# Kernel optimization log

Hardware: AMD Instinct MI355X
Metric: run time of the kernel (lower is better)

Reference implementation:

```python
import jax, jax.numpy as jnp
import numpy as np

EPS = 1e-10
N_NODES = 100000
OUT_CH = 128
N_EDGES = 625000


def setup_inputs() -> dict:
    key = jax.random.key(0)
    k_emb, k_eidx, k_enorm, k_lw, k_sw = jax.random.split(key, 5)
    emb = jax.random.normal(k_emb, (N_NODES, OUT_CH), dtype=jnp.float32) * 0.02
    edge_index = jax.random.randint(k_eidx, (2, N_EDGES), 0, N_NODES, dtype=jnp.int64)
    edge_norm = jax.random.uniform(k_enorm, (N_EDGES,), dtype=jnp.float32)
    scale = 1.0 / np.sqrt(OUT_CH)
    loc_w = jax.random.normal(k_lw, (OUT_CH, OUT_CH), dtype=jnp.float32) * scale
    loc_b = jnp.zeros((OUT_CH,), dtype=jnp.float32)
    std_w = jax.random.normal(k_sw, (OUT_CH, OUT_CH), dtype=jnp.float32) * scale
    std_b = jnp.zeros((OUT_CH,), dtype=jnp.float32)
    return {"emb": emb, "edge_index": edge_index, "edge_norm": edge_norm,
            "loc_w": loc_w, "loc_b": loc_b, "std_w": std_w, "std_b": std_b}


def reference(emb, edge_index, edge_norm, loc_w, loc_b, std_w, std_b):
    """GraphEncoder (GraphConv gather-scale-scatter + Linear loc/std) followed by
    GraphDecoder dot-product logits on the same edge list. Eval mode: z = loc."""
    sidx = edge_index[0]
    tidx = edge_index[1]
    # GraphConv: message = x[sidx] * enorm ; scatter_add into target nodes
    message = emb[sidx] * edge_norm[:, None]               # [E, C]
    ptr = jax.ops.segment_sum(message, tidx, num_segments=emb.shape[0])  # [N, C]
    # Encoder heads (torch Linear: x @ W.T + b)
    loc = ptr @ loc_w.T + loc_b                            # [N, C]
    std = jax.nn.softplus(ptr @ std_w.T + std_b) + EPS     # [N, C]
    z = loc  # eval-mode embedding
    # GraphDecoder: Bernoulli logits per edge
    logits = jnp.sum(z[sidx] * z[tidx], axis=1)            # [E]
    return loc, std, logits
```

## Files before the change

### kernel.cpp

```cpp
#include <hip/hip_runtime.h>

#define N_NODES 100000
#define OUT_CH  128
#define N_EDGES 625000
#define NB_SCAN 98

typedef short short8 __attribute__((ext_vector_type(8)));
typedef float f32x4  __attribute__((ext_vector_type(4)));
typedef float f32x2  __attribute__((ext_vector_type(2)));
typedef unsigned u32x4 __attribute__((ext_vector_type(4)));

__device__ inline short f32_bf16(float f) {
    union { float f; unsigned u; } c{f};
    unsigned r = 0x7FFFu + ((c.u >> 16) & 1u);
    return (short)((c.u + r) >> 16);
}
__device__ inline unsigned pack_bf16x2(float lo, float hi) {
    return (unsigned)(unsigned short)f32_bf16(lo) |
           ((unsigned)(unsigned short)f32_bf16(hi) << 16);
}
__device__ inline float sp_fast(float x) {
    float e = __expf(-fabsf(x));
    return fmaxf(x, 0.f) + __logf(1.f + e);
}

#if defined(__has_builtin)
#if __has_builtin(__builtin_amdgcn_cvt_pk_f32_fp8) && __has_builtin(__builtin_amdgcn_cvt_pk_fp8_f32)
#define HWFP8 1
#endif
#endif
#ifndef HWFP8
#define HWFP8 0
#endif

__device__ inline unsigned f32_fp8_manual(float f) {
    union { float fl; unsigned u; } c{f};
    unsigned s = (c.u >> 31) << 7;
    float af = fabsf(f);
    if (!(af < 448.f)) return s | 0x7E;
    if (af < 0.015625f) {
        unsigned q = (unsigned)__float2int_rn(af * 512.f);
        return s | q;
    }
    unsigned u = c.u;
    u += 0x7FFFF + ((u >> 20) & 1);
    int e = (int)((u >> 23) & 255) - 127;
    if (e > 8) return s | 0x7E;
    return s | (((unsigned)(e + 7)) << 3) | ((u >> 20) & 7);
}
__device__ inline float fp8_f32_manual(unsigned b) {
    unsigned s = (b >> 7) & 1, e = (b >> 3) & 15, m = b & 7;
    if (e) { union { unsigned u; float f; } c{(s << 31) | ((e + 120) << 23) | (m << 20)}; return c.f; }
    float v = (float)m * 0.001953125f;
    return s ? -v : v;
}

template <bool HI>
__device__ inline f32x2 fp8x2_f32(unsigned v) {
#if HWFP8
    return __builtin_amdgcn_cvt_pk_f32_fp8((int)v, HI);
#else
    unsigned sh = HI ? 16 : 0;
    f32x2 r;
    r.x = fp8_f32_manual((v >> sh) & 0xff);
    r.y = fp8_f32_manual((v >> (sh + 8)) & 0xff);
    return r;
#endif
}
template <bool HI>
__device__ inline unsigned fp8_pack2(float a, float b, unsigned old) {
#if HWFP8
    return (unsigned)__builtin_amdgcn_cvt_pk_fp8_f32(a, b, (int)old, HI);
#else
    unsigned v = f32_fp8_manual(a) | (f32_fp8_manual(b) << 8);
    return HI ? ((old & 0x0000ffffu) | (v << 16)) : ((old & 0xffff0000u) | v);
#endif
}

#define NBB 16
#define NBE 6250
#define NBH 2442
__global__ void prep_all(const float* __restrict__ lw, const float* __restrict__ sw,
                         short8* __restrict__ B, const float4* __restrict__ emb,
                         uint2* __restrict__ embf8, const int* __restrict__ ei,
                         int* __restrict__ counts, int use_fp8) {
    int bid = blockIdx.x, tid = threadIdx.x;
    if (bid < NBB) {
        int g = bid * 256 + tid;
        int lane = g & 63, nt = (g >> 6) & 15, ks = g >> 10;
        int c = nt * 16 + (lane & 15);
        int k = ks * 32 + (lane >> 4) * 8;
        const float* src = (c < OUT_CH) ? (lw + c * OUT_CH + k)
                                        : (sw + (c - OUT_CH) * OUT_CH + k);
        short8 o;
#pragma unroll
        for (int j = 0; j < 8; ++j) o[j] = f32_bf16(src[j]);
        B[(ks * 16 + nt) * 64 + lane] = o;
    } else if (bid < NBB + NBE) {
        if (!use_fp8) return;
        int i = (bid - NBB) * 256 + tid;
        float4 a = emb[2 * i], b = emb[2 * i + 1];
        unsigned lo = fp8_pack2<false>(a.x * 64.f, a.y * 64.f, 0u);
        lo = fp8_pack2<true>(a.z * 64.f, a.w * 64.f, lo);
        unsigned hi = fp8_pack2<false>(b.x * 64.f, b.y * 64.f, 0u);
        hi = fp8_pack2<true>(b.z * 64.f, b.w * 64.f, hi);
        uint2 o; o.x = lo; o.y = hi;
        embf8[i] = o;
    } else {
        int e = (bid - NBB - NBE) * 256 + tid;
        if (e < N_EDGES) atomicAdd(&counts[ei[N_EDGES + e]], 1);
    }
}

__global__ void scan1_k(const int* __restrict__ counts, int* __restrict__ offsets,
                        int* __restrict__ partials, int* __restrict__ cursors) {
    __shared__ int wsum[16];
    int tid = threadIdx.x, lane = tid & 63, wid = tid >> 6;
    int e = blockIdx.x * 1024 + tid;
    int v = (e < N_NODES) ? counts[e] : 0;
    int incl = v;
#pragma unroll
    for (int d = 1; d < 64; d <<= 1) {
        int t = __shfl_up(incl, d);
        if (lane >= d) incl += t;
    }
    if (lane == 63) wsum[wid] = incl;
    __syncthreads();
    if (wid == 0) {
        int w = (lane < 16) ? wsum[lane] : 0;
        int wi = w;
#pragma unroll
        for (int d = 1; d < 16; d <<= 1) {
            int t = __shfl_up(wi, d);
            if (lane >= d) wi += t;
        }
        if (lane < 16) wsum[lane] = wi - w;
        if (lane == 15) partials[blockIdx.x] = wi;
    }
    __syncthreads();
    int excl = incl - v + wsum[wid];
    if (e < N_NODES) { offsets[e] = excl; cursors[e] = excl; }
}

__global__ void scan2_k(int* __restrict__ partials, int nb) {
    int lane = threadIdx.x;
    int i0 = 2 * lane, i1 = 2 * lane + 1;
    int v0 = (i0 < nb) ? partials[i0] : 0;
    int v1 = (i1 < nb) ? partials[i1] : 0;
    int s = v0 + v1;
    int incl = s;
#pragma unroll
    for (int d = 1; d < 64; d <<= 1) {
        int t = __shfl_up(incl, d);
        if (lane >= d) incl += t;
    }
    int excl = incl - s;
    if (i0 < nb) partials[i0] = excl;
    if (i1 < nb) partials[i1] = excl + v0;
}

__global__ void reorder_k(const int* __restrict__ ei, const float* __restrict__ en,
                          const int* __restrict__ partials, int* __restrict__ cursors,
                          int4* __restrict__ edata, float nscale) {
    int e = blockIdx.x * blockDim.x + threadIdx.x;
    if (e >= N_EDGES) return;
    int t = ei[N_EDGES + e];
    int pos = partials[t >> 10] + atomicAdd(&cursors[t], 1);
    int4 d;
    d.x = ei[e];
    d.y = __float_as_int(en[e] * nscale);
    d.z = e;
    d.w = t;
    edata[pos] = d;
}

__global__ void gather_fp8_k(const unsigned short* __restrict__ embf8,
                             const int* __restrict__ offsets,
                             const int* __restrict__ partials,
                             const int4* __restrict__ edata,
                             unsigned* __restrict__ ptrb) {
    int g = blockIdx.x * blockDim.x + threadIdx.x;
    int node = __builtin_amdgcn_readfirstlane(g >> 6);
    int lane = threadIdx.x & 63;
    if (node >= N_NODES) return;
    int beg = offsets[node] + partials[node >> 10];
    int end = (node == N_NODES - 1) ? N_EDGES
              : offsets[node + 1] + partials[(node + 1) >> 10];
    float ax = 0.f, ay = 0.f;
    int j = beg;
    for (; j + 4 <= end; j += 4) {
        int4 p0 = edata[j], p1 = edata[j + 1], p2 = edata[j + 2], p3 = edata[j + 3];
        unsigned v0 = embf8[(size_t)p0.x * 64 + lane];
        unsigned v1 = embf8[(size_t)p1.x * 64 + lane];
        unsigned v2 = embf8[(size_t)p2.x * 64 + lane];
        unsigned v3 = embf8[(size_t)p3.x * 64 + lane];
        float n0f = __int_as_float(p0.y), n1f = __int_as_float(p1.y);
        float n2f = __int_as_float(p2.y), n3f = __int_as_float(p3.y);
        f32x2 d0 = fp8x2_f32<false>(v0), d1 = fp8x2_f32<false>(v1);
        f32x2 d2 = fp8x2_f32<false>(v2), d3 = fp8x2_f32<false>(v3);
        ax += d0.x * n0f + d1.x * n1f + d2.x * n2f + d3.x * n3f;
        ay += d0.y * n0f + d1.y * n1f + d2.y * n2f + d3.y * n3f;
    }
    for (; j < end; ++j) {
        int4 p = edata[j];
        float nm = __int_as_float(p.y);
        f32x2 d = fp8x2_f32<false>(embf8[(size_t)p.x * 64 + lane]);
        ax += d.x * nm; ay += d.y * nm;
    }
    ptrb[(size_t)node * 64 + lane] = pack_bf16x2(ax, ay);
}

__global__ void gather_f32_k(const float* __restrict__ emb,
                             const int* __restrict__ offsets,
                             const int* __restrict__ partials,
                             const int4* __restrict__ edata,
                             unsigned* __restrict__ ptrb) {
    int g = blockIdx.x * blockDim.x + threadIdx.x;
    int node = __builtin_amdgcn_readfirstlane(g >> 6);
    int lane = threadIdx.x & 63;
    if (node >= N_NODES) return;
    int beg = offsets[node] + partials[node >> 10];
    int end = (node == N_NODES - 1) ? N_EDGES
              : offsets[node + 1] + partials[(node + 1) >> 10];
    float ax = 0.f, ay = 0.f;
    const float2* base = (const float2*)emb;
    int j = beg;
    for (; j + 4 <= end; j += 4) {
        int4 p0 = edata[j], p1 = edata[j + 1], p2 = edata[j + 2], p3 = edata[j + 3];
        float2 v0 = base[(size_t)p0.x * 64 + lane];
        float2 v1 = base[(size_t)p1.x * 64 + lane];
        float2 v2 = base[(size_t)p2.x * 64 + lane];
        float2 v3 = base[(size_t)p3.x * 64 + lane];
        float n0f = __int_as_float(p0.y), n1f = __int_as_float(p1.y);
        float n2f = __int_as_float(p2.y), n3f = __int_as_float(p3.y);
        ax += v0.x * n0f + v1.x * n1f + v2.x * n2f + v3.x * n3f;
        ay += v0.y * n0f + v1.y * n1f + v2.y * n2f + v3.y * n3f;
    }
    for (; j < end; ++j) {
        int4 p = edata[j];
        float nm = __int_as_float(p.y);
        float2 v = base[(size_t)p.x * 64 + lane];
        ax += v.x * nm; ay += v.y * nm;
    }
    ptrb[(size_t)node * 64 + lane] = pack_bf16x2(ax, ay);
}

__global__ __launch_bounds__(256) void gemm_k(const short* __restrict__ P,
                                              float* __restrict__ out,
                                              const short8* __restrict__ B,
                                              const float* __restrict__ lb,
                                              const float* __restrict__ sb,
                                              unsigned* __restrict__ zf8, int write_z) {
    int tid = threadIdx.x;
    int wave = tid >> 6, lane = tid & 63;
    int n0 = (blockIdx.x * 4 + wave) * 16;
    if (n0 >= N_NODES) return;

    float* loc  = out;
    float* stdo = out + (size_t)N_NODES * OUT_CH;

    int prow = n0 + (lane & 15);
    int kb = (lane >> 4) * 8;

    f32x4 acc[16];
#pragma unroll
    for (int i = 0; i < 16; ++i) acc[i] = (f32x4)(0.f);

#pragma unroll
    for (int ks = 0; ks < 4; ++ks) {
        short8 a = *(const short8*)(P + (size_t)prow * OUT_CH + ks * 32 + kb);
#pragma unroll
        for (int nt = 0; nt < 16; ++nt) {
            short8 w = B[(ks * 16 + nt) * 64 + lane];
            acc[nt] = __builtin_amdgcn_mfma_f32_16x16x32_bf16(w, a, acc[nt], 0, 0, 0);
        }
    }

    int node = n0 + (lane & 15);
    int ch4 = (lane >> 4) * 4;
    float* lrow = loc  + (size_t)node * OUT_CH;
    float* srow = stdo + (size_t)node * OUT_CH;
    unsigned* zrow = zf8 + (size_t)node * 32;

#pragma unroll
    for (int nt = 0; nt < 8; ++nt) {
        int c = nt * 16 + ch4;
        float4 b4 = *(const float4*)(lb + c);
        float4 v;
        v.x = acc[nt][0] + b4.x; v.y = acc[nt][1] + b4.y;
        v.z = acc[nt][2] + b4.z; v.w = acc[nt][3] + b4.w;
        *(float4*)(lrow + c) = v;
        if (write_z) {
            unsigned zp = fp8_pack2<false>(v.x * 16.f, v.y * 16.f, 0u);
            zp = fp8_pack2<true>(v.z * 16.f, v.w * 16.f, zp);
            zrow[c >> 2] = zp;
        }
    }
#pragma unroll
    for (int nt = 8; nt < 16; ++nt) {
        int cc = nt * 16 + ch4 - OUT_CH;
        float4 b4 = *(const float4*)(sb + cc);
        float4 v;
        v.x = sp_fast(acc[nt][0] + b4.x) + 1e-10f;
        v.y = sp_fast(acc[nt][1] + b4.y) + 1e-10f;
        v.z = sp_fast(acc[nt][2] + b4.z) + 1e-10f;
        v.w = sp_fast(acc[nt][3] + b4.w) + 1e-10f;
        *(float4*)(srow + cc) = v;
    }
}

__global__ void logits_fp8_k(const u32x4* __restrict__ zf8,
                             const int4* __restrict__ edata,
                             float* __restrict__ lg) {
    int idx = blockIdx.x * blockDim.x + threadIdx.x;
    int p = idx >> 3, q = idx & 7;
    if (p >= N_EDGES) return;
    int4 md = edata[p];
    u32x4 a = zf8[(size_t)md.x * 8 + q];
    u32x4 b = zf8[(size_t)md.w * 8 + q];
    float d = 0.f;
#pragma unroll
    for (int k = 0; k < 4; ++k) {
        f32x2 al = fp8x2_f32<false>(a[k]), ah = fp8x2_f32<true>(a[k]);
        f32x2 bl = fp8x2_f32<false>(b[k]), bh = fp8x2_f32<true>(b[k]);
        d += al.x * bl.x + al.y * bl.y + ah.x * bh.x + ah.y * bh.y;
    }
#pragma unroll
    for (int m = 4; m >= 1; m >>= 1) d += __shfl_xor(d, m);
    if (q == 0) lg[md.z] = d * 0.00390625f;
}

__global__ void logits_f32_k(const float* __restrict__ z, const int* __restrict__ ei,
                             float* __restrict__ lg) {
    int idx = blockIdx.x * blockDim.x + threadIdx.x;
    int e = idx >> 5, q = idx & 31;
    if (e >= N_EDGES) return;
    int s = ei[e], t = ei[N_EDGES + e];
    float4 a = *(const float4*)(z + (size_t)s * OUT_CH + q * 4);
    float4 b = *(const float4*)(z + (size_t)t * OUT_CH + q * 4);
    float d = a.x * b.x + a.y * b.y + a.z * b.z + a.w * b.w;
#pragma unroll
    for (int m = 16; m >= 1; m >>= 1) d += __shfl_xor(d, m);
    if (q == 0) lg[e] = d;
}

extern "C" void kernel_launch(void* const* d_in, const int* in_sizes, int n_in,
                              void* d_out, int out_size, void* d_ws, size_t ws_size,
                              hipStream_t stream) {
    const float* emb = (const float*)d_in[0];
    const int*   ei  = (const int*)d_in[1];
    const float* en  = (const float*)d_in[2];
    const float* lw  = (const float*)d_in[3];
    const float* lb  = (const float*)d_in[4];
    const float* sw  = (const float*)d_in[5];
    const float* sb  = (const float*)d_in[6];
    float* out = (float*)d_out;

    char* ws = (char*)d_ws;
    size_t o = 0;
    short8* B       = (short8*)(ws + o); o += 65536;
    int*    counts  = (int*)(ws + o);    o += 400128;
    int*    offsets = (int*)(ws + o);    o += 400128;
    int*    cursors = (int*)(ws + o);    o += 400128;
    int*    partials= (int*)(ws + o);    o += 1024;
    int4*   edata   = (int4*)(ws + o);   o += (size_t)N_EDGES * 16;
    unsigned* ptrb  = (unsigned*)(ws + o); o += (size_t)N_NODES * OUT_CH * 2;

    unsigned* zf8   = (unsigned*)(ws + o);
    unsigned short* embf8 = (unsigned short*)(ws + o + (size_t)N_NODES * OUT_CH);
    size_t o_end = o + (size_t)N_NODES * OUT_CH * 2;
    int use_fp8 = (o_end <= ws_size) ? 1 : 0;

    hipMemsetAsync(counts, 0, N_NODES * sizeof(int), stream);

    prep_all<<<NBB + NBE + NBH, 256, 0, stream>>>(lw, sw, B, (const float4*)emb,
                                                  (uint2*)embf8, ei, counts, use_fp8);
    scan1_k<<<NB_SCAN, 1024, 0, stream>>>(counts, offsets, partials, cursors);
    scan2_k<<<1, 64, 0, stream>>>(partials, NB_SCAN);
    reorder_k<<<(N_EDGES + 255) / 256, 256, 0, stream>>>(
        ei, en, partials, cursors, edata, use_fp8 ? 0.015625f : 1.0f);
    if (use_fp8)
        gather_fp8_k<<<(N_NODES * 64 + 255) / 256, 256, 0, stream>>>(
            embf8, offsets, partials, edata, ptrb);
    else
        gather_f32_k<<<(N_NODES * 64 + 255) / 256, 256, 0, stream>>>(
            emb, offsets, partials, edata, ptrb);
    gemm_k<<<(N_NODES / 16 + 3) / 4, 256, 0, stream>>>((const short*)ptrb, out, B,
                                                       lb, sb, zf8, use_fp8);
    float* lg = out + (size_t)2 * N_NODES * OUT_CH;
    if (use_fp8)
        logits_fp8_k<<<((size_t)N_EDGES * 8 + 255) / 256, 256, 0, stream>>>(
            (const u32x4*)zf8, edata, lg);
    else
        logits_f32_k<<<((size_t)N_EDGES * 32 + 255) / 256, 256, 0, stream>>>(out, ei, lg);
}
```

Before: 185.8 us.

## Fuse fp8 neighbor gather with loc/std GEMM through shared memory

Merges the per-node fp8 gather and the bf16 MFMA projection into one kernel. Each 1024-thread block gathers 16 nodes, one per wave, into padded LDS rows, then each of the 16 waves computes one 16-column output tile and writes loc, std and the fp8 z copy. This removes the bf16 intermediate round trip through global memory and one kernel launch. In exchange it adds a block-wide barrier behind the slowest node's gather, and the large blocks may reduce occupancy flexibility.

```diff
diff --git a/kernel.cpp b/kernel.cpp
--- a/kernel.cpp
+++ b/kernel.cpp
@@ -4,6 +4,7 @@
 #define OUT_CH  128
 #define N_EDGES 625000
 #define NB_SCAN 98
+#define ROWD 68
 
 typedef short short8 __attribute__((ext_vector_type(8)));
 typedef float f32x4  __attribute__((ext_vector_type(4)));
@@ -174,15 +175,16 @@
     edata[pos] = d;
 }
 
-__global__ void gather_fp8_k(const unsigned short* __restrict__ embf8,
-                             const int* __restrict__ offsets,
-                             const int* __restrict__ partials,
-                             const int4* __restrict__ edata,
-                             unsigned* __restrict__ ptrb) {
-    int g = blockIdx.x * blockDim.x + threadIdx.x;
-    int node = __builtin_amdgcn_readfirstlane(g >> 6);
-    int lane = threadIdx.x & 63;
-    if (node >= N_NODES) return;
+__global__ __launch_bounds__(1024) void enc_fp8_k(
+        const unsigned short* __restrict__ embf8,
+        const int* __restrict__ offsets, const int* __restrict__ partials,
+        const int4* __restrict__ edata, const short8* __restrict__ B,
+        const float* __restrict__ lb, const float* __restrict__ sb,
+        float* __restrict__ out, unsigned* __restrict__ zf8) {
+    __shared__ unsigned lds[16 * ROWD];
+    int tid = threadIdx.x, wid = tid >> 6, lane = tid & 63;
+    int node = __builtin_amdgcn_readfirstlane(blockIdx.x * 16 + wid);
+
     int beg = offsets[node] + partials[node >> 10];
     int end = (node == N_NODES - 1) ? N_EDGES
               : offsets[node + 1] + partials[(node + 1) >> 10];
@@ -207,7 +209,39 @@
         f32x2 d = fp8x2_f32<false>(embf8[(size_t)p.x * 64 + lane]);
         ax += d.x * nm; ay += d.y * nm;
     }
-    ptrb[(size_t)node * 64 + lane] = pack_bf16x2(ax, ay);
+    lds[wid * ROWD + lane] = pack_bf16x2(ax, ay);
+    __syncthreads();
+
+    int arow = lane & 15, hi = lane >> 4;
+    f32x4 acc = (f32x4)(0.f);
+#pragma unroll
+    for (int ks = 0; ks < 4; ++ks) {
+        short8 a = *(const short8*)&lds[arow * ROWD + ks * 16 + hi * 4];
+        short8 w = B[(ks * 16 + wid) * 64 + lane];
+        acc = __builtin_amdgcn_mfma_f32_16x16x32_bf16(w, a, acc, 0, 0, 0);
+    }
+    int onode = blockIdx.x * 16 + arow;
+    int ch4 = hi * 4;
+    if (wid < 8) {
+        int c = wid * 16 + ch4;
+        float4 b4 = *(const float4*)(lb + c);
+        float4 v;
+        v.x = acc[0] + b4.x; v.y = acc[1] + b4.y;
+        v.z = acc[2] + b4.z; v.w = acc[3] + b4.w;
+        *(float4*)(out + (size_t)onode * OUT_CH + c) = v;
+        unsigned zp = fp8_pack2<false>(v.x * 16.f, v.y * 16.f, 0u);
+        zp = fp8_pack2<true>(v.z * 16.f, v.w * 16.f, zp);
+        zf8[(size_t)onode * 32 + (c >> 2)] = zp;
+    } else {
+        int cc = (wid - 8) * 16 + ch4;
+        float4 b4 = *(const float4*)(sb + cc);
+        float4 v;
+        v.x = sp_fast(acc[0] + b4.x) + 1e-10f;
+        v.y = sp_fast(acc[1] + b4.y) + 1e-10f;
+        v.z = sp_fast(acc[2] + b4.z) + 1e-10f;
+        v.w = sp_fast(acc[3] + b4.w) + 1e-10f;
+        *(float4*)(out + (size_t)N_NODES * OUT_CH + (size_t)onode * OUT_CH + cc) = v;
+    }
 }
 
 __global__ void gather_f32_k(const float* __restrict__ emb,
@@ -249,8 +283,7 @@
                                               float* __restrict__ out,
                                               const short8* __restrict__ B,
                                               const float* __restrict__ lb,
-                                              const float* __restrict__ sb,
-                                              unsigned* __restrict__ zf8, int write_z) {
+                                              const float* __restrict__ sb) {
     int tid = threadIdx.x;
     int wave = tid >> 6, lane = tid & 63;
     int n0 = (blockIdx.x * 4 + wave) * 16;
@@ -280,7 +313,6 @@
     int ch4 = (lane >> 4) * 4;
     float* lrow = loc  + (size_t)node * OUT_CH;
     float* srow = stdo + (size_t)node * OUT_CH;
-    unsigned* zrow = zf8 + (size_t)node * 32;
 
 #pragma unroll
     for (int nt = 0; nt < 8; ++nt) {
@@ -290,11 +322,6 @@
         v.x = acc[nt][0] + b4.x; v.y = acc[nt][1] + b4.y;
         v.z = acc[nt][2] + b4.z; v.w = acc[nt][3] + b4.w;
         *(float4*)(lrow + c) = v;
-        if (write_z) {
-            unsigned zp = fp8_pack2<false>(v.x * 16.f, v.y * 16.f, 0u);
-            zp = fp8_pack2<true>(v.z * 16.f, v.w * 16.f, zp);
-            zrow[c >> 2] = zp;
-        }
     }
 #pragma unroll
     for (int nt = 8; nt < 16; ++nt) {
@@ -379,18 +406,17 @@
     scan2_k<<<1, 64, 0, stream>>>(partials, NB_SCAN);
     reorder_k<<<(N_EDGES + 255) / 256, 256, 0, stream>>>(
         ei, en, partials, cursors, edata, use_fp8 ? 0.015625f : 1.0f);
-    if (use_fp8)
-        gather_fp8_k<<<(N_NODES * 64 + 255) / 256, 256, 0, stream>>>(
-            embf8, offsets, partials, edata, ptrb);
-    else
+    float* lg = out + (size_t)2 * N_NODES * OUT_CH;
+    if (use_fp8) {
+        enc_fp8_k<<<N_NODES / 16, 1024, 0, stream>>>(embf8, offsets, partials,
+                                                     edata, B, lb, sb, out, zf8);
+        logits_fp8_k<<<((size_t)N_EDGES * 8 + 255) / 256, 256, 0, stream>>>(
+            (const u32x4*)zf8, edata, lg);
+    } else {
         gather_f32_k<<<(N_NODES * 64 + 255) / 256, 256, 0, stream>>>(
             emb, offsets, partials, edata, ptrb);
-    gemm_k<<<(N_NODES / 16 + 3) / 4, 256, 0, stream>>>((const short*)ptrb, out, B,
-                                                       lb, sb, zf8, use_fp8);
-    float* lg = out + (size_t)2 * N_NODES * OUT_CH;
-    if (use_fp8)
-        logits_fp8_k<<<((size_t)N_EDGES * 8 + 255) / 256, 256, 0, stream>>>(
-            (const u32x4*)zf8, edata, lg);
-    else
+        gemm_k<<<(N_NODES / 16 + 3) / 4, 256, 0, stream>>>((const short*)ptrb, out,
+                                                           B, lb, sb);
         logits_f32_k<<<((size_t)N_EDGES * 32 + 255) / 256, 256, 0, stream>>>(out, ei, lg);
-}
+    }
+}
```

Result: faster. 177.0 us, median of 2 (-4.7%).
